# Optimization experiments

Hardware: AMD Instinct MI355X
Metric: run time of the kernel (lower is better)

The kernel has to match this reference:

```python
import jax, jax.numpy as jnp
import numpy as np

REST = 0.0
DECAY = 0.2
THRESHOLD = 0.3
BETA = 0.02
SG_WIDTH = 1.0  # rectangular surrogate-gradient window width


@jax.custom_vjp
def spike(v, thresh):
    # forward: hard threshold, y = (v > thresh)
    return (v > thresh).astype(v.dtype)


def _spike_fwd(v, thresh):
    return spike(v, thresh), (v, thresh)


def _spike_bwd(res, g):
    v, thresh = res
    # rectangular surrogate gradient w.r.t. v; threshold gets the negative
    sg = (jnp.abs(v - thresh) < (SG_WIDTH * 0.5)).astype(g.dtype) / SG_WIDTH
    gv = g * sg
    return (gv, -gv)


spike.defvjp(_spike_fwd, _spike_bwd)


def setup_inputs() -> dict:
    key = jax.random.key(0)
    k1, k2 = jax.random.split(key)
    T, B, N = 512, 64, 1024
    tx = jax.random.normal(k1, (T, B, N), dtype=jnp.float32)
    TE = jax.random.normal(k2, (N, T), dtype=jnp.float32) * 0.1  # learned temporal encoding
    return {"tx": tx, "TE": TE}


def reference(tx, TE):
    # tx: [T, B, N] time-major input; TE: [N, T] per-neuron temporal encoding
    T, B, N = tx.shape
    v0 = jnp.full((B, N), REST, tx.dtype)
    y0 = jnp.zeros((B, N), tx.dtype)
    th0 = jnp.full((B, N), THRESHOLD, tx.dtype)

    def step(carry, inp):
        v, y, th = carry
        x, te_t = inp  # x: [B, N], te_t: [N]
        th = th + v * te_t - (th - THRESHOLD) * BETA
        v = v * DECAY * (1.0 - y) + x
        y = spike(v, th)
        return (v, y, th), y

    _, ty = jax.lax.scan(step, (v0, y0, th0), (tx, TE.T))
    return ty  # [T, B, N] spike trains
```

## Files before the change

kernel.cpp:

```cpp
#include <hip/hip_runtime.h>


#define T_STEPS 512
#define BATCH   64
#define NNEUR   1024
#define BN      (BATCH * NNEUR)
#define UCHUNK  16
#define NCHUNK  (T_STEPS / UCHUNK)
#define NSLOT   4
#define CONS_THREADS 256
#define BLOCK_THREADS 320

__global__ __launch_bounds__(BLOCK_THREADS) void telif_kernel(
    const float* __restrict__ tx, const float* __restrict__ TE,
    float* __restrict__ out)
{
#pragma clang fp contract(off)

    __shared__ float buf[NSLOT][UCHUNK][CONS_THREADS];

    const int tid = threadIdx.x;
    const int blockBase = blockIdx.x * CONS_THREADS;

    if (tid >= CONS_THREADS) {
        const int lane = tid - CONS_THREADS;
        const float* gbase = tx + blockBase + lane * 4;

        auto issue_chunk = [&](int k) {
            const int slot = k & (NSLOT - 1);
#pragma unroll
            for (int u = 0; u < UCHUNK; ++u) {
                const float* g = gbase + (size_t)(k * UCHUNK + u) * BN;
                __builtin_amdgcn_global_load_lds(
                    (const __attribute__((address_space(1))) void*)g,
                    (__attribute__((address_space(3))) void*)&buf[slot][u][0],
                    16, 0, 0);
            }
        };

        issue_chunk(0);
        issue_chunk(1);
        issue_chunk(2);
        asm volatile("s_waitcnt vmcnt(32)" ::: "memory");
        __builtin_amdgcn_sched_barrier(0);
        __builtin_amdgcn_s_barrier();

        for (int r = 0; r < NCHUNK; ++r) {
            if (r + 3 < NCHUNK) issue_chunk(r + 3);
            if (r <= NCHUNK - 4) {
                asm volatile("s_waitcnt vmcnt(32)" ::: "memory");
            } else if (r == NCHUNK - 3) {
                asm volatile("s_waitcnt vmcnt(16)" ::: "memory");
            } else {
                asm volatile("s_waitcnt vmcnt(0)" ::: "memory");
            }
            __builtin_amdgcn_sched_barrier(0);
            __builtin_amdgcn_s_barrier();
        }
        return;
    }

    const int flat = blockBase + tid;
    const int n = flat & (NNEUR - 1);
    const float* tep = TE + n * T_STEPS;
    float*       outp = out + flat;

    float v  = 0.0f;
    float y  = 0.0f;
    float th = 0.3f;

    float tc[UCHUNK], tn[UCHUNK];
#pragma unroll
    for (int u = 0; u < UCHUNK; u += 4) {
        float4 f = *reinterpret_cast<const float4*>(tep + u);
        tc[u] = f.x; tc[u + 1] = f.y; tc[u + 2] = f.z; tc[u + 3] = f.w;
    }
    __builtin_amdgcn_s_barrier();

#pragma unroll 1
    for (int r = 0; r < NCHUNK; ++r) {
        const int t = r * UCHUNK;

        if (r + 1 < NCHUNK) {
#pragma unroll
            for (int u = 0; u < UCHUNK; u += 4) {
                float4 f = *reinterpret_cast<const float4*>(tep + t + UCHUNK + u);
                tn[u] = f.x; tn[u + 1] = f.y; tn[u + 2] = f.z; tn[u + 3] = f.w;
            }
        }

        const float* xs = &buf[r & (NSLOT - 1)][0][tid];
#pragma unroll
        for (int u = 0; u < UCHUNK; ++u) {
            float x = xs[(size_t)u * CONS_THREADS];
            float a    = v * tc[u];
            float bsum = th + a;
            float c    = th - 0.3f;
            float d    = c * 0.02f;
            th = bsum - d;
            float e  = v * 0.2f;
            float f1 = 1.0f - y;
            float g  = e * f1;
            v = g + x;
            y = (v > th) ? 1.0f : 0.0f;
            __builtin_nontemporal_store(y, outp + (size_t)(t + u) * BN);
        }

#pragma unroll
        for (int u = 0; u < UCHUNK; ++u) tc[u] = tn[u];

        __builtin_amdgcn_s_barrier();
    }
}

extern "C" void kernel_launch(void* const* d_in, const int* in_sizes, int n_in,
                              void* d_out, int out_size, void* d_ws, size_t ws_size,
                              hipStream_t stream) {
    const float* tx = (const float*)d_in[0];
    const float* TE = (const float*)d_in[1];
    float* out = (float*)d_out;
    telif_kernel<<<BN / CONS_THREADS, BLOCK_THREADS, 0, stream>>>(tx, TE, out);
}
```

Baseline: 233.6 us.

## Drop producer warp, spread async loads across all waves, stage outputs through LDS

Removes the dedicated producer wave. Each of the four compute waves now issues a quarter of the global-to-LDS loads for each chunk, and per-round vmcnt waits are tuned to account for the outstanding output stores. Spike outputs are written to an LDS staging tile, then stored as 16-byte vectorized nontemporal writes, replacing per-thread scalar stores. This adds two block barriers per chunk and more complex vmcnt accounting, which risks stalls or miscounted waits.

```diff
diff --git a/kernel.cpp b/kernel.cpp
--- a/kernel.cpp
+++ b/kernel.cpp
@@ -8,91 +8,90 @@
 #define UCHUNK  16
 #define NCHUNK  (T_STEPS / UCHUNK)
 #define NSLOT   4
-#define CONS_THREADS 256
-#define BLOCK_THREADS 320
+#define DEPTH   3
+#define BT      256
 
-__global__ __launch_bounds__(BLOCK_THREADS) void telif_kernel(
+typedef float f32x4 __attribute__((ext_vector_type(4)));
+
+__global__ __launch_bounds__(BT) void telif_kernel(
     const float* __restrict__ tx, const float* __restrict__ TE,
     float* __restrict__ out)
 {
 #pragma clang fp contract(off)
 
-    __shared__ float buf[NSLOT][UCHUNK][CONS_THREADS];
+    __shared__ float buf[NSLOT][UCHUNK][BT];
+    __shared__ float ystage[UCHUNK][BT];
 
     const int tid = threadIdx.x;
-    const int blockBase = blockIdx.x * CONS_THREADS;
-
-    if (tid >= CONS_THREADS) {
-        const int lane = tid - CONS_THREADS;
-        const float* gbase = tx + blockBase + lane * 4;
-
-        auto issue_chunk = [&](int k) {
-            const int slot = k & (NSLOT - 1);
-#pragma unroll
-            for (int u = 0; u < UCHUNK; ++u) {
-                const float* g = gbase + (size_t)(k * UCHUNK + u) * BN;
-                __builtin_amdgcn_global_load_lds(
-                    (const __attribute__((address_space(1))) void*)g,
-                    (__attribute__((address_space(3))) void*)&buf[slot][u][0],
-                    16, 0, 0);
-            }
-        };
-
-        issue_chunk(0);
-        issue_chunk(1);
-        issue_chunk(2);
-        asm volatile("s_waitcnt vmcnt(32)" ::: "memory");
-        __builtin_amdgcn_sched_barrier(0);
-        __builtin_amdgcn_s_barrier();
-
-        for (int r = 0; r < NCHUNK; ++r) {
-            if (r + 3 < NCHUNK) issue_chunk(r + 3);
-            if (r <= NCHUNK - 4) {
-                asm volatile("s_waitcnt vmcnt(32)" ::: "memory");
-            } else if (r == NCHUNK - 3) {
-                asm volatile("s_waitcnt vmcnt(16)" ::: "memory");
-            } else {
-                asm volatile("s_waitcnt vmcnt(0)" ::: "memory");
-            }
-            __builtin_amdgcn_sched_barrier(0);
-            __builtin_amdgcn_s_barrier();
-        }
-        return;
-    }
-
+    const int wv  = tid >> 6;
+    const int ln  = tid & 63;
+    const int blockBase = blockIdx.x * BT;
     const int flat = blockBase + tid;
     const int n = flat & (NNEUR - 1);
     const float* tep = TE + n * T_STEPS;
-    float*       outp = out + flat;
 
     float v  = 0.0f;
     float y  = 0.0f;
     float th = 0.3f;
 
     float tc[UCHUNK], tn[UCHUNK];
+
+    const float* gld = tx + blockBase + ln * 4;
+
+    auto issue_chunk = [&](int k) {
+        const int slot = k & (NSLOT - 1);
+#pragma unroll
+        for (int j = 0; j < 4; ++j) {
+            const int row = 4 * wv + j;
+            const float* g = gld + (size_t)(k * UCHUNK + row) * BN;
+            __builtin_amdgcn_global_load_lds(
+                (const __attribute__((address_space(1))) void*)g,
+                (__attribute__((address_space(3))) void*)&buf[slot][row][0],
+                16, 0, 0);
+        }
+    };
+
+    issue_chunk(0);
+    issue_chunk(1);
+    issue_chunk(2);
+    __builtin_amdgcn_sched_barrier(0);
 #pragma unroll
     for (int u = 0; u < UCHUNK; u += 4) {
         float4 f = *reinterpret_cast<const float4*>(tep + u);
         tc[u] = f.x; tc[u + 1] = f.y; tc[u + 2] = f.z; tc[u + 3] = f.w;
     }
-    __builtin_amdgcn_s_barrier();
+    __builtin_amdgcn_sched_barrier(0);
 
 #pragma unroll 1
     for (int r = 0; r < NCHUNK; ++r) {
-        const int t = r * UCHUNK;
+        const int t0 = r * UCHUNK;
 
         if (r + 1 < NCHUNK) {
 #pragma unroll
             for (int u = 0; u < UCHUNK; u += 4) {
-                float4 f = *reinterpret_cast<const float4*>(tep + t + UCHUNK + u);
-                tn[u] = f.x; tn[u + 1] = f.y; tn[u + 2] = f.z; tn[u + 3] = f.w;
+                float4 f = *reinterpret_cast<const float4*>(tep + t0 + UCHUNK + u);
+                tn[u] = f.x; tn[u+1] = f.y; tn[u+2] = f.z; tn[u+3] = f.w;
             }
         }
+        __builtin_amdgcn_sched_barrier(0);
 
-        const float* xs = &buf[r & (NSLOT - 1)][0][tid];
+        if (r + DEPTH < NCHUNK) issue_chunk(r + DEPTH);
+        __builtin_amdgcn_sched_barrier(0);
+
+        if (r >= 2 && r <= 28) {
+            asm volatile("s_waitcnt vmcnt(36)" ::: "memory");
+        } else if (r == 1 || r == 30) {
+            asm volatile("s_waitcnt vmcnt(28)" ::: "memory");
+        } else {
+            asm volatile("s_waitcnt vmcnt(20)" ::: "memory");
+        }
+        __builtin_amdgcn_sched_barrier(0);
+        __builtin_amdgcn_s_barrier();
+
+        const float* xcol = &buf[r & (NSLOT - 1)][0][tid];
 #pragma unroll
         for (int u = 0; u < UCHUNK; ++u) {
-            float x = xs[(size_t)u * CONS_THREADS];
+            float x    = xcol[u * BT];
             float a    = v * tc[u];
             float bsum = th + a;
             float c    = th - 0.3f;
@@ -103,13 +102,24 @@
             float g  = e * f1;
             v = g + x;
             y = (v > th) ? 1.0f : 0.0f;
-            __builtin_nontemporal_store(y, outp + (size_t)(t + u) * BN);
+            ystage[u][tid] = y;
         }
+        asm volatile("s_waitcnt lgkmcnt(0)" ::: "memory");
+        __builtin_amdgcn_sched_barrier(0);
+        __builtin_amdgcn_s_barrier();
+
+#pragma unroll
+        for (int j = 0; j < 4; ++j) {
+            const int row = 4 * wv + j;
+            f32x4 yv = *reinterpret_cast<const f32x4*>(&ystage[row][ln * 4]);
+            __builtin_nontemporal_store(yv,
+                reinterpret_cast<f32x4*>(out + (size_t)(t0 + row) * BN
+                                             + blockBase + ln * 4));
+        }
+        __builtin_amdgcn_sched_barrier(0);
 
 #pragma unroll
         for (int u = 0; u < UCHUNK; ++u) tc[u] = tn[u];
-
-        __builtin_amdgcn_s_barrier();
     }
 }
 
@@ -119,5 +129,5 @@
     const float* tx = (const float*)d_in[0];
     const float* TE = (const float*)d_in[1];
     float* out = (float*)d_out;
-    telif_kernel<<<BN / CONS_THREADS, BLOCK_THREADS, 0, stream>>>(tx, TE, out);
+    telif_kernel<<<BN / BT, BT, 0, stream>>>(tx, TE, out);
 }
```

Result: slower. 241.8 us (+3.5%).
